# Optimization experiments

Measured on AMD Instinct MI355X. Metric: run time of the kernel, lower is better.

Reference implementation:

```python
import jax, jax.numpy as jnp
import numpy as np

B, S, DIM, HEADS, DHEAD = 1, 1992, 2048, 16, 128
NKI_SEQ_ALIGN = 128
EPS = 1e-6


def setup_inputs() -> dict:
    key = jax.random.key(0)
    ks = jax.random.split(key, 8)
    hidden_states = jax.random.normal(ks[0], (B, S, DIM), dtype=jnp.float32)
    # realistic rotary tables, full head_dim with interleaved pair angles
    pos = jnp.arange(S, dtype=jnp.float32)
    inv_freq = 1.0 / (10000.0 ** (jnp.arange(0, DHEAD, 2, dtype=jnp.float32) / DHEAD))
    ang = pos[:, None] * inv_freq[None, :]                      # [S, DHEAD/2]
    full = jnp.stack([ang, ang], axis=-1).reshape(S, DHEAD)     # interleave
    freqs_cos = jnp.cos(full)[None, :, None, :]                 # [1,S,1,DHEAD]
    freqs_sin = jnp.sin(full)[None, :, None, :]
    sc = 0.02
    wq = jax.random.normal(ks[1], (DIM, DIM), dtype=jnp.float32) * sc
    wk = jax.random.normal(ks[2], (DIM, DIM), dtype=jnp.float32) * sc
    wv = jax.random.normal(ks[3], (DIM, DIM), dtype=jnp.float32) * sc
    wo = jax.random.normal(ks[4], (DIM, DIM), dtype=jnp.float32) * sc
    bq = jax.random.normal(ks[5], (DIM,), dtype=jnp.float32) * sc
    bk = jax.random.normal(ks[6], (DIM,), dtype=jnp.float32) * sc
    bv = jax.random.normal(ks[7], (DIM,), dtype=jnp.float32) * sc
    bo = jnp.zeros((DIM,), dtype=jnp.float32)
    norm_q_w = jnp.ones((DIM,), dtype=jnp.float32)
    norm_k_w = jnp.ones((DIM,), dtype=jnp.float32)
    return dict(hidden_states=hidden_states, freqs_cos=freqs_cos, freqs_sin=freqs_sin,
                wq=wq, bq=bq, wk=wk, bk=bk, wv=wv, bv=bv,
                norm_q_w=norm_q_w, norm_k_w=norm_k_w, wo=wo, bo=bo)


def _rms_norm(x, weight, eps=EPS):
    xf = x.astype(jnp.float32)
    var = jnp.mean(xf * xf, axis=-1, keepdims=True)
    return (weight * (xf * jax.lax.rsqrt(var + eps))).astype(x.dtype)


def _apply_rope(x, freqs_cos, freqs_sin):
    # x: [B,H,S,D]; freqs: [1,S,1,D]
    cos = jnp.transpose(freqs_cos[..., 0::2], (0, 2, 1, 3))  # [1,1,S,D/2]
    sin = jnp.transpose(freqs_sin[..., 1::2], (0, 2, 1, 3))
    x1, x2 = x[..., 0::2], x[..., 1::2]
    o1 = x1 * cos - x2 * sin
    o2 = x1 * sin + x2 * cos
    return jnp.stack([o1, o2], axis=-1).reshape(x.shape)


def _attention_padded(q, k, v):
    # Faithful to nki_flash_attention: zero-pad seq to multiple of 128,
    # no masking of padded keys (they contribute logit 0), trim query pad.
    B_, H_, S_, D_ = q.shape
    pad = (-S_) % NKI_SEQ_ALIGN
    if pad:
        pc = [(0, 0), (0, 0), (0, pad), (0, 0)]
        q = jnp.pad(q, pc); k = jnp.pad(k, pc); v = jnp.pad(v, pc)
    scale = 1.0 / np.sqrt(D_)
    scores = jnp.einsum('bhqd,bhkd->bhqk', q, k) * scale
    probs = jax.nn.softmax(scores, axis=-1)
    out = jnp.einsum('bhqk,bhkd->bhqd', probs, v)
    return out[:, :, :S_, :]


def reference(hidden_states, freqs_cos, freqs_sin, wq, bq, wk, bk, wv, bv,
              norm_q_w, norm_k_w, wo, bo):
    b, s, _ = hidden_states.shape
    q = hidden_states @ wq.T + bq
    k = hidden_states @ wk.T + bk
    v = hidden_states @ wv.T + bv
    q = _rms_norm(q, norm_q_w)
    k = _rms_norm(k, norm_k_w)
    hd = q.shape[-1] // HEADS
    q = q.reshape(b, s, HEADS, hd).transpose(0, 2, 1, 3)
    k = k.reshape(b, s, HEADS, hd).transpose(0, 2, 1, 3)
    v = v.reshape(b, s, HEADS, hd).transpose(0, 2, 1, 3)
    q = _apply_rope(q, freqs_cos, freqs_sin)
    k = _apply_rope(k, freqs_cos, freqs_sin)
    o = _attention_padded(q, k, v)
    o = o.transpose(0, 2, 1, 3).reshape(b, s, -1)
    return o @ wo.T + bo
```

## Files before the change

kernel.cpp:

```cpp
#include <hip/hip_runtime.h>
#include <cstdint>

#define S_REAL 1992
#define S_PAD  2048
#define DIMSZ  2048
#define NHEAD  16
#define DHD    128

typedef float f32x4 __attribute__((ext_vector_type(4)));
typedef __bf16 bf16x8 __attribute__((ext_vector_type(8)));
typedef unsigned short u16x8 __attribute__((ext_vector_type(8)));

__device__ __forceinline__ unsigned short f2bf(float f){
  uint32_t u = __float_as_uint(f);
  u += 0x7fffu + ((u >> 16) & 1u);
  return (unsigned short)(u >> 16);
}

__device__ __forceinline__ void gload16(const void* g, void* l){
  __builtin_amdgcn_global_load_lds(
      (const __attribute__((address_space(1))) uint32_t*)g,
      (__attribute__((address_space(3))) uint32_t*)l,
      16, 0, 0);
}

template<int N> __device__ __forceinline__ void waitbar(){
  if constexpr (N == 8)      asm volatile("s_waitcnt vmcnt(8)\n\ts_barrier" ::: "memory");
  else if constexpr (N == 6) asm volatile("s_waitcnt vmcnt(6)\n\ts_barrier" ::: "memory");
  else if constexpr (N == 4) asm volatile("s_waitcnt vmcnt(4)\n\ts_barrier" ::: "memory");
  else if constexpr (N == 3) asm volatile("s_waitcnt vmcnt(3)\n\ts_barrier" ::: "memory");
  else if constexpr (N == 2) asm volatile("s_waitcnt vmcnt(2)\n\ts_barrier" ::: "memory");
  else                       asm volatile("s_waitcnt vmcnt(0)\n\ts_barrier" ::: "memory");
}

__launch_bounds__(256)
__global__ void k_cvt5(const float* __restrict__ s0, const float* __restrict__ s1,
                       const float* __restrict__ s2, const float* __restrict__ s3,
                       const float* __restrict__ s4,
                       unsigned short* __restrict__ d0, unsigned short* __restrict__ d1,
                       unsigned short* __restrict__ d2, unsigned short* __restrict__ d3,
                       unsigned short* __restrict__ d4,
                       int nX, int nW)
{
  int i = blockIdx.x * 256 + threadIdx.x;
  const float* s; unsigned short* d; int j;
  if (i < nX){ s = s0; d = d0; j = i; }
  else {
    int k = i - nX;
    int wsel = k / nW; j = k - wsel * nW;
    s = (wsel == 0) ? s1 : (wsel == 1) ? s2 : (wsel == 2) ? s3 : s4;
    d = (wsel == 0) ? d1 : (wsel == 1) ? d2 : (wsel == 2) ? d3 : d4;
  }
  const float4* sp = (const float4*)s + (size_t)j * 2;
  float4 a = sp[0], b = sp[1];
  u16x8 o;
  o[0]=f2bf(a.x); o[1]=f2bf(a.y); o[2]=f2bf(a.z); o[3]=f2bf(a.w);
  o[4]=f2bf(b.x); o[5]=f2bf(b.y); o[6]=f2bf(b.z); o[7]=f2bf(b.w);
  *((u16x8*)d + j) = o;
}

template<int BM, int BN>
__launch_bounds__(256, 2)
__global__ void k_gemm4(const unsigned short* __restrict__ A,
                        const unsigned short* __restrict__ B0,
                        const unsigned short* __restrict__ B1,
                        const unsigned short* __restrict__ B2,
                        const float* __restrict__ bias0,
                        const float* __restrict__ bias1,
                        const float* __restrict__ bias2,
                        float* __restrict__ C0, float* __restrict__ C1, float* __restrict__ C2,
                        int Mreal)
{
  constexpr int AR   = BM / 64;
  constexpr int BR   = BN / 64;
  constexpr int NL   = AR + BR;
  constexpr int WN   = BN / 64;
  constexpr int WM   = 4 / WN;
  constexpr int RM   = BM / WM;
  constexpr int MI   = RM / 16;
  constexpr int BUFE = (BM + BN) * 32;
  constexpr int BOFF = BM * 32;
  constexpr int NT   = DIMSZ / 32;
  constexpr int TN   = DIMSZ / BN;

  __shared__ unsigned short lds[4 * BUFE];

  const unsigned short* Bm = (blockIdx.z == 0) ? B0 : ((blockIdx.z == 1) ? B1 : B2);
  const float* bias        = (blockIdx.z == 0) ? bias0 : ((blockIdx.z == 1) ? bias1 : bias2);
  float* C                 = (blockIdx.z == 0) ? C0 : ((blockIdx.z == 1) ? C1 : C2);

  const int fid = blockIdx.x + gridDim.x * blockIdx.y;
  const int q   = (gridDim.x * gridDim.y) >> 3;
  const int nf  = (fid & 7) * q + (fid >> 3);
  const int m0  = (nf / TN) * BM, n0 = (nf % TN) * BN;

  const int tid = threadIdx.x;
  const int w = tid >> 6, l = tid & 63;
  const int lr = l & 15, lg = l >> 4;
  const int wr = (w / WN) * RM, wc = (w % WN) * 64;

  f32x4 acc[MI][4];
  #pragma unroll
  for (int mi = 0; mi < MI; ++mi)
    #pragma unroll
    for (int ni = 0; ni < 4; ++ni)
      acc[mi][ni] = (f32x4){0.f, 0.f, 0.f, 0.f};

#define G8_STAGE(TT) do{                                                          \
    const int k0s = (TT) * 32;                                                    \
    unsigned short* dst = &lds[((TT) & 3) * BUFE];                                \
    _Pragma("unroll")                                                             \
    for (int i_ = 0; i_ < AR; ++i_){                                              \
      int lin = i_ * 256 + tid;                                                   \
      int r_ = lin >> 2, pos_ = lin & 3;                                          \
      int gr_ = m0 + r_; if (gr_ > Mreal - 1) gr_ = Mreal - 1;                    \
      gload16(A + (size_t)gr_ * DIMSZ + k0s + (pos_ ^ ((r_ >> 1) & 3)) * 8,       \
              dst + lin * 8);                                                     \
    }                                                                             \
    _Pragma("unroll")                                                             \
    for (int i_ = 0; i_ < BR; ++i_){                                              \
      int lin = i_ * 256 + tid;                                                   \
      int r_ = lin >> 2, pos_ = lin & 3;                                          \
      gload16(Bm + (size_t)(n0 + r_) * DIMSZ + k0s + (pos_ ^ ((r_ >> 1) & 3)) * 8,\
              dst + BOFF + lin * 8);                                              \
    }                                                                             \
  } while(0)

#define G8_COMPUTE(TT) do{                                                        \
    const unsigned short* sb = &lds[((TT) & 3) * BUFE];                           \
    bf16x8 af_[MI]; bf16x8 bf_[4];                                                \
    _Pragma("unroll")                                                             \
    for (int mi = 0; mi < MI; ++mi){                                              \
      int r_ = wr + mi * 16 + lr;                                                 \
      af_[mi] = *(const bf16x8*)(sb + r_ * 32 + (lg ^ ((r_ >> 1) & 3)) * 8);      \
    }                                                                             \
    _Pragma("unroll")                                                             \
    for (int ni = 0; ni < 4; ++ni){                                               \
      int r_ = wc + ni * 16 + lr;                                                 \
      bf_[ni] = *(const bf16x8*)(sb + BOFF + r_ * 32 + (lg ^ ((r_ >> 1) & 3)) * 8);\
    }                                                                             \
    __builtin_amdgcn_s_setprio(1);                                                \
    _Pragma("unroll")                                                             \
    for (int mi = 0; mi < MI; ++mi)                                               \
      _Pragma("unroll")                                                           \
      for (int ni = 0; ni < 4; ++ni)                                              \
        acc[mi][ni] = __builtin_amdgcn_mfma_f32_16x16x32_bf16(af_[mi], bf_[ni],   \
                                                              acc[mi][ni], 0, 0, 0);\
    __builtin_amdgcn_s_setprio(0);                                                \
  } while(0)

  G8_STAGE(0); G8_STAGE(1); G8_STAGE(2);

  for (int tt = 0; tt < NT - 3; ++tt){
    waitbar<2 * NL>();
    G8_STAGE(tt + 3);
    G8_COMPUTE(tt);
  }
  waitbar<2 * NL>(); G8_COMPUTE(NT - 3);
  waitbar<NL>();     G8_COMPUTE(NT - 2);
  waitbar<0>();      G8_COMPUTE(NT - 1);

#undef G8_STAGE
#undef G8_COMPUTE

  #pragma unroll
  for (int ni = 0; ni < 4; ++ni){
    int col = n0 + wc + ni * 16 + lr;
    float bz = bias[col];
    #pragma unroll
    for (int mi = 0; mi < MI; ++mi){
      #pragma unroll
      for (int j = 0; j < 4; ++j){
        int row = m0 + wr + mi * 16 + lg * 4 + j;
        if (row < Mreal) C[(size_t)row * DIMSZ + col] = acc[mi][ni][j] + bz;
      }
    }
  }
}

__launch_bounds__(256)
__global__ void k_normrope2(const float* __restrict__ Qf, const float* __restrict__ Kf,
                            const float* __restrict__ nqw, const float* __restrict__ nkw,
                            const float* __restrict__ fc, const float* __restrict__ fs,
                            unsigned short* __restrict__ OutQ, unsigned short* __restrict__ OutK)
{
  const int s = blockIdx.x;
  const int isK = blockIdx.y;
  const float* Xf = isK ? Kf : Qf;
  const float* nw = isK ? nkw : nqw;
  unsigned short* Out = isK ? OutK : OutQ;
  const float scale = isK ? 1.0f : 0.08838834764831843f;
  const int swz = isK;

  const int t = threadIdx.x;
  const int w = t >> 6, l = t & 63;
  __shared__ float wred[4];
  float v[8];
  float ss = 0.f;
  if (s < S_REAL){
    const float4* p = (const float4*)(Xf + (size_t)s * DIMSZ) + t * 2;
    float4 a = p[0], b = p[1];
    v[0]=a.x; v[1]=a.y; v[2]=a.z; v[3]=a.w; v[4]=b.x; v[5]=b.y; v[6]=b.z; v[7]=b.w;
    #pragma unroll
    for (int j = 0; j < 8; ++j) ss += v[j] * v[j];
  }
  #pragma unroll
  for (int off = 32; off >= 1; off >>= 1) ss += __shfl_xor(ss, off);
  if (l == 0) wred[w] = ss;
  __syncthreads();
  float tot = wred[0] + wred[1] + wred[2] + wred[3];
  float rinv = rsqrtf(tot * (1.f / DIMSZ) + 1e-6f);

  const int h  = t >> 4;
  const int d0 = (t & 15) * 8;
  const int b  = t & 15;
  const int bsw = swz ? (b ^ (s & 7)) : b;
  unsigned short* dst = Out + ((size_t)h * S_PAD + s) * DHD + bsw * 8;
  u16x8 o;
  if (s < S_REAL){
    #pragma unroll
    for (int i = 0; i < 4; ++i){
      float c_ = fc[s * DHD + d0 + 2 * i];
      float s_ = fs[s * DHD + d0 + 2 * i + 1];
      float x1 = v[2 * i]     * rinv * nw[t * 8 + 2 * i];
      float x2 = v[2 * i + 1] * rinv * nw[t * 8 + 2 * i + 1];
      o[2 * i]     = f2bf((x1 * c_ - x2 * s_) * scale);
      o[2 * i + 1] = f2bf((x1 * s_ + x2 * c_) * scale);
    }
  } else {
    #pragma unroll
    for (int j = 0; j < 8; ++j) o[j] = 0;
  }
  *(u16x8*)dst = o;
}

__launch_bounds__(256)
__global__ void k_vtrans(const float* __restrict__ Vf, unsigned short* __restrict__ Vth)
{
  __shared__ unsigned short tile[64][72];
  const int t = threadIdx.x;
  const int s0 = blockIdx.x * 64, c0 = blockIdx.y * 64;
  #pragma unroll
  for (int i = 0; i < 4; ++i){
    int r = (t >> 4) * 4 + i;
    int s = s0 + r;
    int cq = (t & 15) * 4;
    float4 val = {0.f, 0.f, 0.f, 0.f};
    if (s < S_REAL) val = *((const float4*)(Vf + (size_t)s * DIMSZ + c0) + (t & 15));
    tile[r][cq + 0] = f2bf(val.x);
    tile[r][cq + 1] = f2bf(val.y);
    tile[r][cq + 2] = f2bf(val.z);
    tile[r][cq + 3] = f2bf(val.w);
  }
  __syncthreads();
  const int cl = t >> 2;
  const int cc = c0 + cl;
  #pragma unroll
  for (int bi = 0; bi < 2; ++bi){
    int b = (t & 3) * 2 + bi;
    u16x8 o;
    #pragma unroll
    for (int j = 0; j < 8; ++j) o[j] = tile[b * 8 + j][cl];
    int bsw = b ^ (cc & 7);
    *(u16x8*)(Vth + (size_t)cc * S_PAD + s0 + bsw * 8) = o;
  }
}

__launch_bounds__(256)
__global__ void k_attn(const unsigned short* __restrict__ Qh,
                       const unsigned short* __restrict__ Kh,
                       const unsigned short* __restrict__ Vth,
                       unsigned short* __restrict__ O)
{
  __shared__ unsigned short kbuf[2][64 * 128];
  __shared__ unsigned short vbuf[2][128 * 64];
  __shared__ unsigned short pbuf[4][16 * 64];
  const int h = blockIdx.y;
  const int q0 = blockIdx.x * 64;
  const int t = threadIdx.x, w = t >> 6, l = t & 63;
  const int lr = l & 15, lg = l >> 4;

  const unsigned short* Qp = Qh + ((size_t)h * S_PAD + q0 + w * 16 + lr) * DHD;
  bf16x8 qf[4];
  #pragma unroll
  for (int ks = 0; ks < 4; ++ks) qf[ks] = *(const bf16x8*)(Qp + ks * 32 + lg * 8);

  f32x4 acc[8];
  #pragma unroll
  for (int nf = 0; nf < 8; ++nf) acc[nf] = (f32x4){0.f, 0.f, 0.f, 0.f};
  float m = -3.0e38f, lsum = 0.f;

#define ATT_STAGE(KT, BI) do{                                                       \
    _Pragma("unroll")                                                               \
    for (int i_ = 0; i_ < 4; ++i_){                                                 \
      int rK = (w * 4 + i_) * 4 + (l >> 4);                                         \
      gload16(Kh + ((size_t)h * S_PAD + (KT) * 64 + rK) * DHD + (l & 15) * 8,       \
              &kbuf[BI][(w * 4 + i_) * 512]);                                       \
      int rV = (w * 4 + i_) * 8 + (l >> 3);                                         \
      gload16(Vth + ((size_t)h * DHD + rV) * S_PAD + (KT) * 64 + (l & 7) * 8,       \
              &vbuf[BI][(w * 4 + i_) * 512]);                                       \
    }                                                                               \
  } while(0)

  ATT_STAGE(0, 0);
  __syncthreads();

  for (int kt = 0; kt < S_PAD / 64; ++kt){
    const int bi = kt & 1;
    if (kt < S_PAD / 64 - 1) ATT_STAGE(kt + 1, bi ^ 1);

    f32x4 sf[4];
    __builtin_amdgcn_s_setprio(1);
    #pragma unroll
    for (int kvf = 0; kvf < 4; ++kvf){
      sf[kvf] = (f32x4){0.f, 0.f, 0.f, 0.f};
      int r = kvf * 16 + lr;
      #pragma unroll
      for (int ks = 0; ks < 4; ++ks){
        int blk = (ks * 4 + lg) ^ (r & 7);
        bf16x8 kf = *(const bf16x8*)&kbuf[bi][r * 128 + blk * 8];
        sf[kvf] = __builtin_amdgcn_mfma_f32_16x16x32_bf16(kf, qf[ks], sf[kvf], 0, 0, 0);
      }
    }
    __builtin_amdgcn_s_setprio(0);

    float pmax = sf[0][0];
    #pragma unroll
    for (int kvf = 0; kvf < 4; ++kvf)
      #pragma unroll
      for (int j = 0; j < 4; ++j) pmax = fmaxf(pmax, sf[kvf][j]);
    pmax = fmaxf(pmax, __shfl_xor(pmax, 16));
    pmax = fmaxf(pmax, __shfl_xor(pmax, 32));
    float mn = fmaxf(m, pmax);
    float fr = __expf(m - mn);
    m = mn;
    float p[4][4];
    float psum = 0.f;
    #pragma unroll
    for (int kvf = 0; kvf < 4; ++kvf)
      #pragma unroll
      for (int j = 0; j < 4; ++j){ p[kvf][j] = __expf(sf[kvf][j] - mn); psum += p[kvf][j]; }
    lsum = lsum * fr + psum;

    float fv0 = __shfl(fr, lg * 4 + 0);
    float fv1 = __shfl(fr, lg * 4 + 1);
    float fv2 = __shfl(fr, lg * 4 + 2);
    float fv3 = __shfl(fr, lg * 4 + 3);
    f32x4 fv = (f32x4){fv0, fv1, fv2, fv3};
    #pragma unroll
    for (int nf = 0; nf < 8; ++nf) acc[nf] *= fv;

    char* pb = (char*)pbuf[w];
    #pragma unroll
    for (int kvf = 0; kvf < 4; ++kvf){
      uint2 wv;
      wv.x = (uint32_t)f2bf(p[kvf][0]) | ((uint32_t)f2bf(p[kvf][1]) << 16);
      wv.y = (uint32_t)f2bf(p[kvf][2]) | ((uint32_t)f2bf(p[kvf][3]) << 16);
      int byte = lr * 128 + (((kvf * 2 + (lg >> 1)) ^ (lr & 7)) * 16) + (lg & 1) * 8;
      *(uint2*)(pb + byte) = wv;
    }
    bf16x8 pf[2];
    #pragma unroll
    for (int c = 0; c < 2; ++c)
      pf[c] = *(const bf16x8*)(pb + lr * 128 + ((c * 4 + lg) ^ (lr & 7)) * 16);

    __builtin_amdgcn_s_setprio(1);
    #pragma unroll
    for (int nf = 0; nf < 8; ++nf){
      int cc = nf * 16 + lr;
      #pragma unroll
      for (int ks = 0; ks < 2; ++ks){
        int blk = (ks * 4 + lg) ^ (cc & 7);
        bf16x8 vf = *(const bf16x8*)&vbuf[bi][cc * 64 + blk * 8];
        acc[nf] = __builtin_amdgcn_mfma_f32_16x16x32_bf16(pf[ks], vf, acc[nf], 0, 0, 0);
      }
    }
    __builtin_amdgcn_s_setprio(0);

    __syncthreads();
  }
#undef ATT_STAGE

  lsum += __shfl_xor(lsum, 16);
  lsum += __shfl_xor(lsum, 32);
  float ls0 = __shfl(lsum, lg * 4 + 0);
  float ls1 = __shfl(lsum, lg * 4 + 1);
  float ls2 = __shfl(lsum, lg * 4 + 2);
  float ls3 = __shfl(lsum, lg * 4 + 3);
  f32x4 lsv = (f32x4){1.f / ls0, 1.f / ls1, 1.f / ls2, 1.f / ls3};

  #pragma unroll
  for (int nf = 0; nf < 8; ++nf){
    #pragma unroll
    for (int j = 0; j < 4; ++j){
      int row = q0 + w * 16 + lg * 4 + j;
      if (row < S_REAL)
        O[(size_t)row * DIMSZ + h * DHD + nf * 16 + lr] = f2bf(acc[nf][j] * lsv[j]);
    }
  }
}

extern "C" void kernel_launch(void* const* d_in, const int* in_sizes, int n_in,
                              void* d_out, int out_size, void* d_ws, size_t ws_size,
                              hipStream_t stream)
{
  const float* hidden = (const float*)d_in[0];
  const float* fc  = (const float*)d_in[1];
  const float* fs  = (const float*)d_in[2];
  const float* wq  = (const float*)d_in[3];
  const float* bq  = (const float*)d_in[4];
  const float* wk  = (const float*)d_in[5];
  const float* bk  = (const float*)d_in[6];
  const float* wv  = (const float*)d_in[7];
  const float* bv  = (const float*)d_in[8];
  const float* nqw = (const float*)d_in[9];
  const float* nkw = (const float*)d_in[10];
  const float* wo  = (const float*)d_in[11];
  const float* bo  = (const float*)d_in[12];
  float* out = (float*)d_out;

  char* ws = (char*)d_ws;
  size_t off = 0;
  auto alloc = [&](size_t bytes) -> void* {
    void* p = ws + off;
    off += (bytes + 255) & ~(size_t)255;
    return p;
  };
  unsigned short* Xb  = (unsigned short*)alloc((size_t)S_REAL * DIMSZ * 2);
  unsigned short* Wqb = (unsigned short*)alloc((size_t)DIMSZ * DIMSZ * 2);
  unsigned short* Wkb = (unsigned short*)alloc((size_t)DIMSZ * DIMSZ * 2);
  unsigned short* Wvb = (unsigned short*)alloc((size_t)DIMSZ * DIMSZ * 2);
  unsigned short* Wob = (unsigned short*)alloc((size_t)DIMSZ * DIMSZ * 2);
  float* Qf = (float*)alloc((size_t)S_REAL * DIMSZ * 4);
  float* Kf = (float*)alloc((size_t)S_REAL * DIMSZ * 4);
  float* Vf = (float*)alloc((size_t)S_REAL * DIMSZ * 4);
  unsigned short* Qhh = (unsigned short*)alloc((size_t)NHEAD * S_PAD * DHD * 2);
  unsigned short* Khh = (unsigned short*)alloc((size_t)NHEAD * S_PAD * DHD * 2);
  unsigned short* Vth = (unsigned short*)alloc((size_t)NHEAD * DHD * S_PAD * 2);
  unsigned short* Oa  = (unsigned short*)alloc((size_t)S_REAL * DIMSZ * 2);

  {
    int nX = S_REAL * DIMSZ / 8;
    int nW = DIMSZ * DIMSZ / 8;
    int total = nX + 4 * nW;
    k_cvt5<<<total / 256, 256, 0, stream>>>(hidden, wq, wk, wv, wo,
                                            Xb, Wqb, Wkb, Wvb, Wob, nX, nW);
  }

  k_gemm4<128, 128><<<dim3(16, 16, 3), 256, 0, stream>>>(Xb, Wqb, Wkb, Wvb, bq, bk, bv,
                                                         Qf, Kf, Vf, S_REAL);

  k_normrope2<<<dim3(S_PAD, 2), 256, 0, stream>>>(Qf, Kf, nqw, nkw, fc, fs, Qhh, Khh);

  k_vtrans<<<dim3(S_PAD / 64, DIMSZ / 64), 256, 0, stream>>>(Vf, Vth);

  k_attn<<<dim3(S_PAD / 64, NHEAD), 256, 0, stream>>>(Qhh, Khh, Vth, Oa);

  k_gemm4<128, 64><<<dim3(16, 32, 1), 256, 0, stream>>>(Oa, Wob, Wob, Wob, bo, bo, bo,
                                                        out, out, out, S_REAL);
}
```

Measured before the change: 221.8 us.

## Switch projection GEMMs to 32x32x16 MFMA with triple-buffered LDS pipeline

Replaces the templated GEMM with a fixed 128x128 tile kernel that uses 32x32x16 bf16 MFMA instructions instead of 16x16x32, cutting LDS fragment reads per MFMA. The LDS pipeline drops from four to three buffers, which raises the occupancy hint to 3 blocks per CU. The output projection now also uses 128x128 tiles (256 blocks instead of 512). The risks are fewer blocks for the output GEMM, so less parallelism, and a shallower prefetch depth.

```diff
diff --git a/kernel.cpp b/kernel.cpp
--- a/kernel.cpp
+++ b/kernel.cpp
@@ -8,6 +8,7 @@
 #define DHD    128
 
 typedef float f32x4 __attribute__((ext_vector_type(4)));
+typedef float f32x16 __attribute__((ext_vector_type(16)));
 typedef __bf16 bf16x8 __attribute__((ext_vector_type(8)));
 typedef unsigned short u16x8 __attribute__((ext_vector_type(8)));
 
@@ -59,31 +60,20 @@
   *((u16x8*)d + j) = o;
 }
 
-template<int BM, int BN>
-__launch_bounds__(256, 2)
-__global__ void k_gemm4(const unsigned short* __restrict__ A,
-                        const unsigned short* __restrict__ B0,
-                        const unsigned short* __restrict__ B1,
-                        const unsigned short* __restrict__ B2,
-                        const float* __restrict__ bias0,
-                        const float* __restrict__ bias1,
-                        const float* __restrict__ bias2,
-                        float* __restrict__ C0, float* __restrict__ C1, float* __restrict__ C2,
-                        int Mreal)
-{
-  constexpr int AR   = BM / 64;
-  constexpr int BR   = BN / 64;
-  constexpr int NL   = AR + BR;
-  constexpr int WN   = BN / 64;
-  constexpr int WM   = 4 / WN;
-  constexpr int RM   = BM / WM;
-  constexpr int MI   = RM / 16;
-  constexpr int BUFE = (BM + BN) * 32;
-  constexpr int BOFF = BM * 32;
+__launch_bounds__(256, 3)
+__global__ void k_g32(const unsigned short* __restrict__ A,
+                      const unsigned short* __restrict__ B0,
+                      const unsigned short* __restrict__ B1,
+                      const unsigned short* __restrict__ B2,
+                      const float* __restrict__ bias0,
+                      const float* __restrict__ bias1,
+                      const float* __restrict__ bias2,
+                      float* __restrict__ C0, float* __restrict__ C1, float* __restrict__ C2,
+                      int Mreal)
+{
+  constexpr int BUFE = 8192;
   constexpr int NT   = DIMSZ / 32;
-  constexpr int TN   = DIMSZ / BN;
-
-  __shared__ unsigned short lds[4 * BUFE];
+  __shared__ unsigned short lds[3 * BUFE];
 
   const unsigned short* Bm = (blockIdx.z == 0) ? B0 : ((blockIdx.z == 1) ? B1 : B2);
   const float* bias        = (blockIdx.z == 0) ? bias0 : ((blockIdx.z == 1) ? bias1 : bias2);
@@ -92,25 +82,26 @@
   const int fid = blockIdx.x + gridDim.x * blockIdx.y;
   const int q   = (gridDim.x * gridDim.y) >> 3;
   const int nf  = (fid & 7) * q + (fid >> 3);
-  const int m0  = (nf / TN) * BM, n0 = (nf % TN) * BN;
+  const int m0  = (nf >> 4) * 128, n0 = (nf & 15) * 128;
 
   const int tid = threadIdx.x;
   const int w = tid >> 6, l = tid & 63;
-  const int lr = l & 15, lg = l >> 4;
-  const int wr = (w / WN) * RM, wc = (w % WN) * 64;
-
-  f32x4 acc[MI][4];
-  #pragma unroll
-  for (int mi = 0; mi < MI; ++mi)
-    #pragma unroll
-    for (int ni = 0; ni < 4; ++ni)
-      acc[mi][ni] = (f32x4){0.f, 0.f, 0.f, 0.f};
-
-#define G8_STAGE(TT) do{                                                          \
+  const int l31 = l & 31, l5 = l >> 5;
+  const int wr = (w >> 1) * 64, wc = (w & 1) * 64;
+
+  f32x16 acc[2][2];
+  #pragma unroll
+  for (int mb = 0; mb < 2; ++mb)
+    #pragma unroll
+    for (int nb = 0; nb < 2; ++nb)
+      #pragma unroll
+      for (int r = 0; r < 16; ++r) acc[mb][nb][r] = 0.f;
+
+#define G32_STAGE(TT, BASE) do{                                                   \
     const int k0s = (TT) * 32;                                                    \
-    unsigned short* dst = &lds[((TT) & 3) * BUFE];                                \
+    unsigned short* dst = (BASE);                                                 \
     _Pragma("unroll")                                                             \
-    for (int i_ = 0; i_ < AR; ++i_){                                              \
+    for (int i_ = 0; i_ < 2; ++i_){                                               \
       int lin = i_ * 256 + tid;                                                   \
       int r_ = lin >> 2, pos_ = lin & 3;                                          \
       int gr_ = m0 + r_; if (gr_ > Mreal - 1) gr_ = Mreal - 1;                    \
@@ -118,61 +109,74 @@
               dst + lin * 8);                                                     \
     }                                                                             \
     _Pragma("unroll")                                                             \
-    for (int i_ = 0; i_ < BR; ++i_){                                              \
+    for (int i_ = 0; i_ < 2; ++i_){                                               \
       int lin = i_ * 256 + tid;                                                   \
       int r_ = lin >> 2, pos_ = lin & 3;                                          \
       gload16(Bm + (size_t)(n0 + r_) * DIMSZ + k0s + (pos_ ^ ((r_ >> 1) & 3)) * 8,\
-              dst + BOFF + lin * 8);                                              \
+              dst + 4096 + lin * 8);                                              \
     }                                                                             \
   } while(0)
 
-#define G8_COMPUTE(TT) do{                                                        \
-    const unsigned short* sb = &lds[((TT) & 3) * BUFE];                           \
-    bf16x8 af_[MI]; bf16x8 bf_[4];                                                \
+#define G32_COMPUTE(BASE) do{                                                     \
+    const unsigned short* sb = (BASE);                                            \
+    bf16x8 a_[2][2], b_[2][2];                                                    \
     _Pragma("unroll")                                                             \
-    for (int mi = 0; mi < MI; ++mi){                                              \
-      int r_ = wr + mi * 16 + lr;                                                 \
-      af_[mi] = *(const bf16x8*)(sb + r_ * 32 + (lg ^ ((r_ >> 1) & 3)) * 8);      \
-    }                                                                             \
+    for (int mb = 0; mb < 2; ++mb)                                                \
+      _Pragma("unroll")                                                           \
+      for (int ks = 0; ks < 2; ++ks){                                             \
+        int r_ = wr + mb * 32 + l31;                                              \
+        int c_ = (ks * 2 + l5) ^ ((r_ >> 1) & 3);                                 \
+        a_[mb][ks] = *(const bf16x8*)(sb + r_ * 32 + c_ * 8);                     \
+      }                                                                           \
     _Pragma("unroll")                                                             \
-    for (int ni = 0; ni < 4; ++ni){                                               \
-      int r_ = wc + ni * 16 + lr;                                                 \
-      bf_[ni] = *(const bf16x8*)(sb + BOFF + r_ * 32 + (lg ^ ((r_ >> 1) & 3)) * 8);\
-    }                                                                             \
+    for (int nb = 0; nb < 2; ++nb)                                                \
+      _Pragma("unroll")                                                           \
+      for (int ks = 0; ks < 2; ++ks){                                             \
+        int r_ = wc + nb * 32 + l31;                                              \
+        int c_ = (ks * 2 + l5) ^ ((r_ >> 1) & 3);                                 \
+        b_[nb][ks] = *(const bf16x8*)(sb + 4096 + r_ * 32 + c_ * 8);              \
+      }                                                                           \
     __builtin_amdgcn_s_setprio(1);                                                \
     _Pragma("unroll")                                                             \
-    for (int mi = 0; mi < MI; ++mi)                                               \
+    for (int ks = 0; ks < 2; ++ks)                                                \
       _Pragma("unroll")                                                           \
-      for (int ni = 0; ni < 4; ++ni)                                              \
-        acc[mi][ni] = __builtin_amdgcn_mfma_f32_16x16x32_bf16(af_[mi], bf_[ni],   \
-                                                              acc[mi][ni], 0, 0, 0);\
+      for (int mb = 0; mb < 2; ++mb)                                              \
+        _Pragma("unroll")                                                         \
+        for (int nb = 0; nb < 2; ++nb)                                            \
+          acc[mb][nb] = __builtin_amdgcn_mfma_f32_32x32x16_bf16(a_[mb][ks],       \
+                            b_[nb][ks], acc[mb][nb], 0, 0, 0);                    \
     __builtin_amdgcn_s_setprio(0);                                                \
   } while(0)
 
-  G8_STAGE(0); G8_STAGE(1); G8_STAGE(2);
-
-  for (int tt = 0; tt < NT - 3; ++tt){
-    waitbar<2 * NL>();
-    G8_STAGE(tt + 3);
-    G8_COMPUTE(tt);
-  }
-  waitbar<2 * NL>(); G8_COMPUTE(NT - 3);
-  waitbar<NL>();     G8_COMPUTE(NT - 2);
-  waitbar<0>();      G8_COMPUTE(NT - 1);
-
-#undef G8_STAGE
-#undef G8_COMPUTE
-
-  #pragma unroll
-  for (int ni = 0; ni < 4; ++ni){
-    int col = n0 + wc + ni * 16 + lr;
+  G32_STAGE(0, lds);
+  G32_STAGE(1, lds + BUFE);
+  int bc = 0, bs = 2;
+  for (int tt = 0; tt < NT - 2; ++tt){
+    waitbar<4>();
+    G32_STAGE(tt + 2, lds + bs * BUFE);
+    G32_COMPUTE(lds + bc * BUFE);
+    bs = (bs == 2) ? 0 : bs + 1;
+    bc = (bc == 2) ? 0 : bc + 1;
+  }
+  waitbar<4>();
+  G32_COMPUTE(lds + bc * BUFE);
+  bc = (bc == 2) ? 0 : bc + 1;
+  waitbar<0>();
+  G32_COMPUTE(lds + bc * BUFE);
+
+#undef G32_STAGE
+#undef G32_COMPUTE
+
+  #pragma unroll
+  for (int nb = 0; nb < 2; ++nb){
+    int col = n0 + wc + nb * 32 + l31;
     float bz = bias[col];
     #pragma unroll
-    for (int mi = 0; mi < MI; ++mi){
-      #pragma unroll
-      for (int j = 0; j < 4; ++j){
-        int row = m0 + wr + mi * 16 + lg * 4 + j;
-        if (row < Mreal) C[(size_t)row * DIMSZ + col] = acc[mi][ni][j] + bz;
+    for (int mb = 0; mb < 2; ++mb){
+      #pragma unroll
+      for (int r = 0; r < 16; ++r){
+        int row = m0 + wr + mb * 32 + (r & 3) + 8 * (r >> 2) + 4 * l5;
+        if (row < Mreal) C[(size_t)row * DIMSZ + col] = acc[mb][nb][r] + bz;
       }
     }
   }
@@ -447,8 +451,8 @@
                                             Xb, Wqb, Wkb, Wvb, Wob, nX, nW);
   }
 
-  k_gemm4<128, 128><<<dim3(16, 16, 3), 256, 0, stream>>>(Xb, Wqb, Wkb, Wvb, bq, bk, bv,
-                                                         Qf, Kf, Vf, S_REAL);
+  k_g32<<<dim3(16, 16, 3), 256, 0, stream>>>(Xb, Wqb, Wkb, Wvb, bq, bk, bv,
+                                             Qf, Kf, Vf, S_REAL);
 
   k_normrope2<<<dim3(S_PAD, 2), 256, 0, stream>>>(Qf, Kf, nqw, nkw, fc, fs, Qhh, Khh);
 
@@ -456,6 +460,6 @@
 
   k_attn<<<dim3(S_PAD / 64, NHEAD), 256, 0, stream>>>(Qhh, Khh, Vth, Oa);
 
-  k_gemm4<128, 64><<<dim3(16, 32, 1), 256, 0, stream>>>(Oa, Wob, Wob, Wob, bo, bo, bo,
-                                                        out, out, out, S_REAL);
-}
+  k_g32<<<dim3(16, 16, 1), 256, 0, stream>>>(Oa, Wob, Wob, Wob, bo, bo, bo,
+                                             out, out, out, S_REAL);
+}
```

Measured after the change: 220.0 us. About the same (-0.8%).
